# Kernel optimization log

Hardware: AMD Instinct MI355X
Metric: run time of the kernel (lower is better)

Reference implementation:

```python
import jax, jax.numpy as jnp
import numpy as np
import math

INPUT_SIZE = 1024
HIDDEN_SIZE = 1024
RANK = 256
BATCH = 32
SEQ = 512


def setup_inputs() -> dict:
    key = jax.random.key(0)
    k_x, k_a, k_b, k_c = jax.random.split(key, 4)
    stdv = 1.0 / math.sqrt(HIDDEN_SIZE)
    x = jax.random.normal(k_x, (BATCH, SEQ, INPUT_SIZE), dtype=jnp.float32)
    a = jax.random.uniform(k_a, (HIDDEN_SIZE, RANK * 4), minval=-stdv, maxval=stdv, dtype=jnp.float32)
    b = jax.random.uniform(k_b, (INPUT_SIZE, RANK * 4), minval=-stdv, maxval=stdv, dtype=jnp.float32)
    ct = jax.random.uniform(k_c, (RANK * 4, HIDDEN_SIZE), minval=-stdv, maxval=stdv, dtype=jnp.float32)
    return {"x": x, "a": a, "b": b, "ct": ct}


def reference(x, a, b, ct):
    B, S, _ = x.shape
    H = a.shape[0]
    R = a.shape[1] // 4
    ct3 = ct.reshape(4, R, H)  # (4, R, H)
    # Precompute input projection for all timesteps: (B, S, 4R)
    xb = jnp.einsum('bsi,ir->bsr', x, b)

    def step(carry, xb_t):
        h, c = carry
        g = (h @ a) * xb_t                      # (B, 4R)
        g = jnp.einsum('bkr,krh->bkh', g.reshape(B, 4, R), ct3)  # (B, 4, H)
        f_t = jax.nn.sigmoid(g[:, 0])
        i_t = jax.nn.sigmoid(g[:, 1])
        g_t = jnp.tanh(g[:, 2])
        o_t = jax.nn.sigmoid(g[:, 3])
        c = f_t * c + i_t * g_t
        h = o_t * jnp.tanh(c)
        return (h, c), h

    h0 = jnp.zeros((B, H), dtype=x.dtype)
    c0 = jnp.zeros((B, H), dtype=x.dtype)
    (h_t, c_t), hs = jax.lax.scan(step, (h0, c0), jnp.swapaxes(xb, 0, 1))
    hidden_seq = jnp.swapaxes(hs, 0, 1)  # (B, S, H)
    return hidden_seq, (h_t, c_t)
```

## Files before the change

### kernel.cpp

```cpp
#include <hip/hip_runtime.h>
#include <math.h>

#define NTHR 512

__device__ __forceinline__ void st_uc(float* p, float v) {
    asm volatile("global_store_dword %0, %1, off sc0 sc1" :: "v"(p), "v"(v) : "memory");
}
__device__ __forceinline__ void st_uc_u(unsigned* p, unsigned v) {
    asm volatile("global_store_dword %0, %1, off sc0 sc1" :: "v"(p), "v"(v) : "memory");
}
__device__ __forceinline__ float4 ld_uc4_nw(const float4* p) {
    float4 v;
    asm volatile("global_load_dwordx4 %0, %1, off sc0 sc1" : "=v"(v) : "v"(p) : "memory");
    return v;
}
__device__ __forceinline__ float ld_uc_nw(const float* p) {
    float v;
    asm volatile("global_load_dword %0, %1, off sc0 sc1" : "=v"(v) : "v"(p) : "memory");
    return v;
}
__device__ __forceinline__ void spin_tags64(const unsigned* base, int L, unsigned target) {
    const unsigned* p = base + L;
    for (;;) {
        unsigned v;
        asm volatile("global_load_dword %0, %1, off sc0 sc1\n\ts_waitcnt vmcnt(0)"
                     : "=v"(v) : "v"(p) : "memory");
        if (!__any((int)(v < target))) return;
        __builtin_amdgcn_s_sleep(1);
    }
}

__global__ void init_kernel(float* h_buf, unsigned* tags) {
    int i = blockIdx.x * blockDim.x + threadIdx.x;
    if (i < 65536) st_uc(h_buf + i, 0.0f);
    if (i < 1024) st_uc_u(tags + i, 0u);
}

__global__ __launch_bounds__(256) void xb_gemm(const float* __restrict__ X,
                                               const float* __restrict__ Bw,
                                               float* __restrict__ XB) {
    __shared__ float xs[16][132];
    __shared__ float bs[16][132];
    const int bm = blockIdx.x >> 3;
    const int bn = blockIdx.x & 7;
    const int m0 = bm * 128, n0 = bn * 128;
    const int tid = threadIdx.x;
    const int tx = tid & 15, ty = tid >> 4;
    float acc[8][8];
#pragma unroll
    for (int i = 0; i < 8; ++i)
#pragma unroll
        for (int j = 0; j < 8; ++j) acc[i][j] = 0.f;

    for (int k0 = 0; k0 < 1024; k0 += 16) {
#pragma unroll
        for (int p = 0; p < 2; ++p) {
            int f = tid + p * 256;
            int m = f >> 2, kq = f & 3;
            float4 v = *(const float4*)&X[(size_t)(m0 + m) * 1024 + k0 + kq * 4];
            xs[kq * 4 + 0][m] = v.x; xs[kq * 4 + 1][m] = v.y;
            xs[kq * 4 + 2][m] = v.z; xs[kq * 4 + 3][m] = v.w;
        }
#pragma unroll
        for (int p = 0; p < 2; ++p) {
            int f = tid + p * 256;
            int k = f >> 5, n = (f & 31) * 4;
            float4 v = *(const float4*)&Bw[(size_t)(k0 + k) * 1024 + n0 + n];
            *(float4*)&bs[k][n] = v;
        }
        __syncthreads();
#pragma unroll
        for (int k = 0; k < 16; ++k) {
            float xv[8], bv[8];
            *(float4*)&xv[0] = *(const float4*)&xs[k][ty * 8];
            *(float4*)&xv[4] = *(const float4*)&xs[k][ty * 8 + 4];
            *(float4*)&bv[0] = *(const float4*)&bs[k][tx * 8];
            *(float4*)&bv[4] = *(const float4*)&bs[k][tx * 8 + 4];
#pragma unroll
            for (int i = 0; i < 8; ++i)
#pragma unroll
                for (int j = 0; j < 8; ++j) acc[i][j] += xv[i] * bv[j];
        }
        __syncthreads();
    }
#pragma unroll
    for (int i = 0; i < 8; ++i)
#pragma unroll
        for (int j = 0; j < 8; j += 4) {
            float4 v = make_float4(acc[i][j], acc[i][j + 1], acc[i][j + 2], acc[i][j + 3]);
            *(float4*)&XB[(size_t)(m0 + ty * 8 + i) * 1024 + n0 + tx * 8 + j] = v;
        }
}

__global__ __launch_bounds__(NTHR, 1) void scan_kernel(
    const float* __restrict__ A, const float* __restrict__ CTm,
    float* __restrict__ XBH, float* __restrict__ h_buf, float* __restrict__ g_buf,
    float* __restrict__ ht_out, float* __restrict__ ct_out, unsigned* __restrict__ tags) {
    extern __shared__ float lds[];
    float* a_lf  = lds;
    float* ct_lf = lds + 16384;
    float* st0f  = lds + 32768;
    float* st1f  = lds + 36864;
    float4* lds4  = (float4*)lds;
    const float4* a_l4  = lds4;
    const float4* ct_l4 = lds4 + 4096;
    float4* st0_4 = lds4 + 8192;
    float4* st1_4 = lds4 + 9216;
    float* scr0 = st0f;
    float* scr1 = st1f;

    const int wg = blockIdx.x;
    const int bg0 = wg >> 6;
    const int bg1 = bg0 + 4;
    const int sg = wg & 63;
    const int c0wg = sg * 16;
    const int tid = threadIdx.x;

    {
        const int c = tid & 15, i0 = tid >> 4;
        for (int i = i0; i < 1024; i += 32) {
            a_lf[c * 1024 + i]  = A[(size_t)i * 1024 + c0wg + c];
            ct_lf[c * 1024 + i] = CTm[(size_t)i * 1024 + c0wg + c];
        }
    }

    const int L  = tid & 63;
    const int w  = tid >> 6;
    const int Lc = L & 7;
    const int Lb = (L >> 3) & 3;
    const int cg = w & 1, kq = w >> 1;

    int wIdx[8], sIdx[4];
#pragma unroll
    for (int c = 0; c < 8; ++c) wIdx[c] = (cg * 8 + (c ^ Lc)) * 256 + kq * 64 + L;
#pragma unroll
    for (int r = 0; r < 4; ++r) sIdx[r] = ((r ^ Lb) << 8) + kq * 64 + L;

    const int e_b   = L >> 4;
    const int e_j   = L & 15;
    const int e_cgo = e_j >> 3;
    const int e_sx  = e_b * 8 + (e_j & 7);
    const int col   = c0wg + e_j;

    float4* h4 = (float4*)h_buf;
    float4* g4 = (float4*)g_buf;

    float creg = 0.f;
    __syncthreads();

    auto sub = [&](int t, const unsigned* pollbase, unsigned polltgt,
                   const float4* src4, float4* st4, float* scr,
                   const float4* wmat, int epiw, bool isA, int bgx, float xbv) {
        if (w == 7) spin_tags64(pollbase, L, polltgt);
        __syncthreads();
        {
            float4 u0 = ld_uc4_nw(src4 + tid);
            float4 u1 = ld_uc4_nw(src4 + 512 + tid);
            asm volatile("s_waitcnt vmcnt(0)" ::: "memory");
            __builtin_amdgcn_sched_barrier(0);
            st4[tid] = u0; st4[512 + tid] = u1;
        }
        __syncthreads();
        float v[32];
        {
            float4 sv[4], wv[8];
#pragma unroll
            for (int r = 0; r < 4; ++r) sv[r] = st4[sIdx[r]];
#pragma unroll
            for (int c = 0; c < 8; ++c) wv[c] = wmat[wIdx[c]];
#pragma unroll
            for (int r = 0; r < 4; ++r)
#pragma unroll
                for (int c = 0; c < 8; ++c)
                    v[r * 8 + c] = sv[r].x * wv[c].x + sv[r].y * wv[c].y
                                 + sv[r].z * wv[c].z + sv[r].w * wv[c].w;
        }
#pragma unroll
        for (int j = 0; j < 16; ++j) v[j] = v[2 * j] + __shfl_xor(v[2 * j + 1], 1);
#pragma unroll
        for (int j = 0; j < 8; ++j)  v[j] = v[2 * j] + __shfl_xor(v[2 * j + 1], 2);
#pragma unroll
        for (int j = 0; j < 4; ++j)  v[j] = v[2 * j] + __shfl_xor(v[2 * j + 1], 4);
#pragma unroll
        for (int j = 0; j < 2; ++j)  v[j] = v[2 * j] + __shfl_xor(v[2 * j + 1], 8);
        v[0] = v[0] + __shfl_xor(v[1], 16);
        v[0] = v[0] + __shfl_xor(v[0], 32);
        __syncthreads();
        if (L < 32) scr[kq * 64 + cg * 32 + L] = v[0];
        __syncthreads();
        if (w == epiw) {
            asm volatile("s_waitcnt vmcnt(0)" ::: "memory");
            const int bglob = bgx * 4 + e_b;
            float q0 = scr[e_cgo * 32 + e_sx];
            float q1 = scr[64 + e_cgo * 32 + e_sx];
            float q2 = scr[128 + e_cgo * 32 + e_sx];
            float q3 = scr[192 + e_cgo * 32 + e_sx];
            if (isA) {
                float gv = (q0 + q1 + q2 + q3) * xbv;
                st_uc(g_buf + (t & 1) * 32768 + (size_t)bglob * 1024 + col, gv);
                asm volatile("s_waitcnt vmcnt(0)" ::: "memory");
                if (L == 0) st_uc_u(tags + bgx * 128 + 64 + sg, (unsigned)t + 1u);
            } else {
                float ft = 1.f / (1.f + __expf(-q0));
                float it = 1.f / (1.f + __expf(-q1));
                float gt = tanhf(q2);
                float ot = 1.f / (1.f + __expf(-q3));
                creg = ft * creg + it * gt;
                float hv = ot * tanhf(creg);
                st_uc(h_buf + (t & 1) * 32768 + (size_t)bglob * 1024 + col, hv);
                st_uc(XBH + ((size_t)bglob * 512 + t) * 1024 + col, hv);
                if (t == 511) {
                    st_uc(ht_out + (size_t)bglob * 1024 + col, hv);
                    st_uc(ct_out + (size_t)bglob * 1024 + col, creg);
                }
                asm volatile("s_waitcnt vmcnt(0)" ::: "memory");
                if (L == 0) st_uc_u(tags + bgx * 128 + sg, (unsigned)t + 1u);
            }
        }
    };

    for (int t = 0; t < 512; ++t) {
        const unsigned tu = (unsigned)t;
        float xb0 = 0.f, xb1 = 0.f;
        if (w == 0) xb0 = ld_uc_nw(XBH + ((size_t)(bg0 * 4 + e_b) * 512 + t) * 1024 + col);
        if (w == 4) xb1 = ld_uc_nw(XBH + ((size_t)(bg1 * 4 + e_b) * 512 + t) * 1024 + col);

        sub(t, tags + bg0 * 128, tu,
            h4 + ((t + 1) & 1) * 8192 + bg0 * 1024, st0_4, scr0, a_l4, 0, true, bg0, xb0);
        sub(t, tags + bg1 * 128, tu,
            h4 + ((t + 1) & 1) * 8192 + bg1 * 1024, st1_4, scr1, a_l4, 4, true, bg1, xb1);
        sub(t, tags + bg0 * 128 + 64, tu + 1u,
            g4 + (t & 1) * 8192 + bg0 * 1024, st0_4, scr0, ct_l4, 0, false, bg0, 0.f);
        sub(t, tags + bg1 * 128 + 64, tu + 1u,
            g4 + (t & 1) * 8192 + bg1 * 1024, st1_4, scr1, ct_l4, 4, false, bg1, 0.f);
    }
}

extern "C" void kernel_launch(void* const* d_in, const int* in_sizes, int n_in,
                              void* d_out, int out_size, void* d_ws, size_t ws_size,
                              hipStream_t stream) {
    const float* X   = (const float*)d_in[0];
    const float* A   = (const float*)d_in[1];
    const float* Bw  = (const float*)d_in[2];
    const float* CTm = (const float*)d_in[3];

    float* out    = (float*)d_out;
    float* XBH    = out;
    float* ht_out = out + (size_t)32 * 512 * 1024;
    float* ct_out = ht_out + 32 * 1024;

    float* h_buf = (float*)d_ws;
    float* g_buf = h_buf + 65536;
    unsigned* tags = (unsigned*)(g_buf + 65536);

    (void)hipFuncSetAttribute((const void*)scan_kernel,
                              hipFuncAttributeMaxDynamicSharedMemorySize, 163840);

    init_kernel<<<dim3(256), dim3(256), 0, stream>>>(h_buf, tags);
    xb_gemm<<<dim3(1024), dim3(256), 0, stream>>>(X, Bw, XBH);
    scan_kernel<<<dim3(256), dim3(NTHR), 163840, stream>>>(A, CTm, XBH, h_buf, g_buf,
                                                           ht_out, ct_out, tags);
}
```

Baseline: 4.868 ms.

## Software-pipeline scan substeps: prefetch next state during current matvec

Restructures the persistent scan loop so that the two batch groups' phases are interleaved (A0, B1 of previous step, B0, A1). Each substep polls and prefetches the next operand from global memory while the current LDS matvec runs. A single staging buffer is used and barriers are reduced. This targets the serialized poll→load→compute latency on every substep. In exchange the ordering is more complex, with a prologue and epilogue, which risks correctness or deadlock subtleties.

```diff
diff --git a/kernel.cpp b/kernel.cpp
--- a/kernel.cpp
+++ b/kernel.cpp
@@ -19,16 +19,7 @@
     asm volatile("global_load_dword %0, %1, off sc0 sc1" : "=v"(v) : "v"(p) : "memory");
     return v;
 }
-__device__ __forceinline__ void spin_tags64(const unsigned* base, int L, unsigned target) {
-    const unsigned* p = base + L;
-    for (;;) {
-        unsigned v;
-        asm volatile("global_load_dword %0, %1, off sc0 sc1\n\ts_waitcnt vmcnt(0)"
-                     : "=v"(v) : "v"(p) : "memory");
-        if (!__any((int)(v < target))) return;
-        __builtin_amdgcn_s_sleep(1);
-    }
-}
+#define VMCNT0 asm volatile("s_waitcnt vmcnt(0)" ::: "memory")
 
 __global__ void init_kernel(float* h_buf, unsigned* tags) {
     int i = blockIdx.x * blockDim.x + threadIdx.x;
@@ -99,22 +90,23 @@
     extern __shared__ float lds[];
     float* a_lf  = lds;
     float* ct_lf = lds + 16384;
-    float* st0f  = lds + 32768;
-    float* st1f  = lds + 36864;
-    float4* lds4  = (float4*)lds;
-    const float4* a_l4  = lds4;
-    const float4* ct_l4 = lds4 + 4096;
-    float4* st0_4 = lds4 + 8192;
-    float4* st1_4 = lds4 + 9216;
-    float* scr0 = st0f;
-    float* scr1 = st1f;
-
-    const int wg = blockIdx.x;
+    float* stgf  = lds + 32768;
+    float* scr0  = lds + 36864;
+    float* scr1  = lds + 37120;
+    const float4* a_l4  = (const float4*)a_lf;
+    const float4* ct_l4 = (const float4*)ct_lf;
+    float4* stg4 = (float4*)stgf;
+
+    const int wg  = blockIdx.x;
     const int bg0 = wg >> 6;
     const int bg1 = bg0 + 4;
-    const int sg = wg & 63;
+    const int sg  = wg & 63;
     const int c0wg = sg * 16;
     const int tid = threadIdx.x;
+    unsigned* tagH0 = tags + bg0 * 128;
+    unsigned* tagG0 = tagH0 + 64;
+    unsigned* tagH1 = tags + bg1 * 128;
+    unsigned* tagG1 = tagH1 + 64;
 
     {
         const int c = tid & 15, i0 = tid >> 4;
@@ -136,45 +128,50 @@
 #pragma unroll
     for (int r = 0; r < 4; ++r) sIdx[r] = ((r ^ Lb) << 8) + kq * 64 + L;
 
+    const int stag = (tid & 255) >> 2;
+
     const int e_b   = L >> 4;
     const int e_j   = L & 15;
     const int e_cgo = e_j >> 3;
     const int e_sx  = e_b * 8 + (e_j & 7);
     const int col   = c0wg + e_j;
 
-    float4* h4 = (float4*)h_buf;
-    float4* g4 = (float4*)g_buf;
+    const float4* h4 = (const float4*)h_buf;
+    const float4* g4 = (const float4*)g_buf;
 
     float creg = 0.f;
-    __syncthreads();
-
-    auto sub = [&](int t, const unsigned* pollbase, unsigned polltgt,
-                   const float4* src4, float4* st4, float* scr,
-                   const float4* wmat, int epiw, bool isA, int bgx, float xbv) {
-        if (w == 7) spin_tags64(pollbase, L, polltgt);
-        __syncthreads();
-        {
-            float4 u0 = ld_uc4_nw(src4 + tid);
-            float4 u1 = ld_uc4_nw(src4 + 512 + tid);
-            asm volatile("s_waitcnt vmcnt(0)" ::: "memory");
-            __builtin_amdgcn_sched_barrier(0);
-            st4[tid] = u0; st4[512 + tid] = u1;
-        }
-        __syncthreads();
+    float xbv = 0.f;
+    float4 pr0, pr1;
+
+    auto poll = [&](const unsigned* base, unsigned tgt) {
+        const unsigned* p = base + stag;
+        for (;;) {
+            unsigned vv;
+            asm volatile("global_load_dword %0, %1, off sc0 sc1\n\ts_waitcnt vmcnt(0)"
+                         : "=v"(vv) : "v"(p) : "memory");
+            if (!__any((int)(vv < tgt))) return;
+            __builtin_amdgcn_s_sleep(1);
+        }
+    };
+    auto subcore = [&](const float4* wmat, float* scr,
+                       const unsigned* pfb, unsigned pft, const float4* pfsrc, bool dopf) {
+        float4 sv[4], wv[8];
+#pragma unroll
+        for (int r = 0; r < 4; ++r) sv[r] = stg4[sIdx[r]];
+#pragma unroll
+        for (int c = 0; c < 8; ++c) wv[c] = wmat[wIdx[c]];
+        if (dopf) {
+            poll(pfb, pft);
+            pr0 = ld_uc4_nw(pfsrc + tid);
+            pr1 = ld_uc4_nw(pfsrc + 512 + tid);
+        }
         float v[32];
-        {
-            float4 sv[4], wv[8];
-#pragma unroll
-            for (int r = 0; r < 4; ++r) sv[r] = st4[sIdx[r]];
-#pragma unroll
-            for (int c = 0; c < 8; ++c) wv[c] = wmat[wIdx[c]];
-#pragma unroll
-            for (int r = 0; r < 4; ++r)
-#pragma unroll
-                for (int c = 0; c < 8; ++c)
-                    v[r * 8 + c] = sv[r].x * wv[c].x + sv[r].y * wv[c].y
-                                 + sv[r].z * wv[c].z + sv[r].w * wv[c].w;
-        }
+#pragma unroll
+        for (int r = 0; r < 4; ++r)
+#pragma unroll
+            for (int c = 0; c < 8; ++c)
+                v[r * 8 + c] = sv[r].x * wv[c].x + sv[r].y * wv[c].y
+                             + sv[r].z * wv[c].z + sv[r].w * wv[c].w;
 #pragma unroll
         for (int j = 0; j < 16; ++j) v[j] = v[2 * j] + __shfl_xor(v[2 * j + 1], 1);
 #pragma unroll
@@ -185,55 +182,106 @@
         for (int j = 0; j < 2; ++j)  v[j] = v[2 * j] + __shfl_xor(v[2 * j + 1], 8);
         v[0] = v[0] + __shfl_xor(v[1], 16);
         v[0] = v[0] + __shfl_xor(v[0], 32);
-        __syncthreads();
         if (L < 32) scr[kq * 64 + cg * 32 + L] = v[0];
-        __syncthreads();
-        if (w == epiw) {
-            asm volatile("s_waitcnt vmcnt(0)" ::: "memory");
-            const int bglob = bgx * 4 + e_b;
-            float q0 = scr[e_cgo * 32 + e_sx];
-            float q1 = scr[64 + e_cgo * 32 + e_sx];
-            float q2 = scr[128 + e_cgo * 32 + e_sx];
-            float q3 = scr[192 + e_cgo * 32 + e_sx];
-            if (isA) {
-                float gv = (q0 + q1 + q2 + q3) * xbv;
-                st_uc(g_buf + (t & 1) * 32768 + (size_t)bglob * 1024 + col, gv);
-                asm volatile("s_waitcnt vmcnt(0)" ::: "memory");
-                if (L == 0) st_uc_u(tags + bgx * 128 + 64 + sg, (unsigned)t + 1u);
+    };
+    auto epiA = [&](int t, float* scrS, int bgx, unsigned* tagGx) {
+        VMCNT0;
+        float q = scrS[e_cgo * 32 + e_sx] + scrS[64 + e_cgo * 32 + e_sx]
+                + scrS[128 + e_cgo * 32 + e_sx] + scrS[192 + e_cgo * 32 + e_sx];
+        st_uc(g_buf + (t & 1) * 32768 + (size_t)(bgx * 4 + e_b) * 1024 + col, q * xbv);
+        VMCNT0;
+        if (L == 0) st_uc_u(tagGx + sg, (unsigned)t + 1u);
+    };
+    auto epiB = [&](int t, float* scrS, int bgx, unsigned* tagHx) {
+        float q0 = scrS[e_cgo * 32 + e_sx],       q1 = scrS[64 + e_cgo * 32 + e_sx];
+        float q2 = scrS[128 + e_cgo * 32 + e_sx], q3 = scrS[192 + e_cgo * 32 + e_sx];
+        float ft = 1.f / (1.f + __expf(-q0));
+        float it = 1.f / (1.f + __expf(-q1));
+        float gt = tanhf(q2);
+        float ot = 1.f / (1.f + __expf(-q3));
+        creg = ft * creg + it * gt;
+        float hv = ot * tanhf(creg);
+        int bglob = bgx * 4 + e_b;
+        st_uc(h_buf + (t & 1) * 32768 + (size_t)bglob * 1024 + col, hv);
+        st_uc(XBH + ((size_t)bglob * 512 + t) * 1024 + col, hv);
+        if (t == 511) {
+            st_uc(ht_out + (size_t)bglob * 1024 + col, hv);
+            st_uc(ct_out + (size_t)bglob * 1024 + col, creg);
+        }
+        VMCNT0;
+        if (L == 0) st_uc_u(tagHx + sg, (unsigned)t + 1u);
+    };
+
+    __syncthreads();
+    {
+        const float4* s = h4 + 8192 + (size_t)bg0 * 1024;
+        pr0 = ld_uc4_nw(s + tid);
+        pr1 = ld_uc4_nw(s + 512 + tid);
+        VMCNT0;
+        stg4[tid] = pr0; stg4[512 + tid] = pr1;
+        __syncthreads();
+    }
+
+    for (int k = 0; k < 512; ++k) {
+        if (w == 1) xbv = ld_uc_nw(XBH + ((size_t)(bg0 * 4 + e_b) * 512 + k) * 1024 + col);
+        if (w == 2) xbv = ld_uc_nw(XBH + ((size_t)(bg1 * 4 + e_b) * 512 + k) * 1024 + col);
+
+        subcore(a_l4, scr0, tagG1, (unsigned)k,
+                g4 + ((k + 1) & 1) * 8192 + (size_t)bg1 * 1024, true);
+        __syncthreads();
+        if (w == 1) epiA(k, scr0, bg0, tagG0);
+        VMCNT0;
+        stg4[tid] = pr0; stg4[512 + tid] = pr1;
+        __syncthreads();
+
+        {
+            const float4* srcn = g4 + (k & 1) * 8192 + (size_t)bg0 * 1024;
+            if (k > 0) {
+                subcore(ct_l4, scr1, tagG0, (unsigned)k + 1u, srcn, true);
             } else {
-                float ft = 1.f / (1.f + __expf(-q0));
-                float it = 1.f / (1.f + __expf(-q1));
-                float gt = tanhf(q2);
-                float ot = 1.f / (1.f + __expf(-q3));
-                creg = ft * creg + it * gt;
-                float hv = ot * tanhf(creg);
-                st_uc(h_buf + (t & 1) * 32768 + (size_t)bglob * 1024 + col, hv);
-                st_uc(XBH + ((size_t)bglob * 512 + t) * 1024 + col, hv);
-                if (t == 511) {
-                    st_uc(ht_out + (size_t)bglob * 1024 + col, hv);
-                    st_uc(ct_out + (size_t)bglob * 1024 + col, creg);
-                }
-                asm volatile("s_waitcnt vmcnt(0)" ::: "memory");
-                if (L == 0) st_uc_u(tags + bgx * 128 + sg, (unsigned)t + 1u);
+                poll(tagG0, 1u);
+                pr0 = ld_uc4_nw(srcn + tid);
+                pr1 = ld_uc4_nw(srcn + 512 + tid);
             }
-        }
-    };
-
-    for (int t = 0; t < 512; ++t) {
-        const unsigned tu = (unsigned)t;
-        float xb0 = 0.f, xb1 = 0.f;
-        if (w == 0) xb0 = ld_uc_nw(XBH + ((size_t)(bg0 * 4 + e_b) * 512 + t) * 1024 + col);
-        if (w == 4) xb1 = ld_uc_nw(XBH + ((size_t)(bg1 * 4 + e_b) * 512 + t) * 1024 + col);
-
-        sub(t, tags + bg0 * 128, tu,
-            h4 + ((t + 1) & 1) * 8192 + bg0 * 1024, st0_4, scr0, a_l4, 0, true, bg0, xb0);
-        sub(t, tags + bg1 * 128, tu,
-            h4 + ((t + 1) & 1) * 8192 + bg1 * 1024, st1_4, scr1, a_l4, 4, true, bg1, xb1);
-        sub(t, tags + bg0 * 128 + 64, tu + 1u,
-            g4 + (t & 1) * 8192 + bg0 * 1024, st0_4, scr0, ct_l4, 0, false, bg0, 0.f);
-        sub(t, tags + bg1 * 128 + 64, tu + 1u,
-            g4 + (t & 1) * 8192 + bg1 * 1024, st1_4, scr1, ct_l4, 4, false, bg1, 0.f);
-    }
+            __syncthreads();
+            if (k > 0 && w == 4) epiB(k - 1, scr1, bg1, tagH1);
+            VMCNT0;
+            stg4[tid] = pr0; stg4[512 + tid] = pr1;
+            __syncthreads();
+        }
+
+        subcore(ct_l4, scr0, tagH1, (unsigned)k,
+                h4 + ((k + 1) & 1) * 8192 + (size_t)bg1 * 1024, true);
+        __syncthreads();
+        if (w == 0) epiB(k, scr0, bg0, tagH0);
+        VMCNT0;
+        stg4[tid] = pr0; stg4[512 + tid] = pr1;
+        __syncthreads();
+
+        {
+            bool pf = (k < 511);
+            subcore(a_l4, scr1, tagH0, (unsigned)k + 1u,
+                    h4 + (k & 1) * 8192 + (size_t)bg0 * 1024, pf);
+            __syncthreads();
+            if (w == 2) epiA(k, scr1, bg1, tagG1);
+            VMCNT0;
+            if (pf) { stg4[tid] = pr0; stg4[512 + tid] = pr1; }
+            __syncthreads();
+        }
+    }
+
+    poll(tagG1, 512u);
+    {
+        const float4* s = g4 + 8192 + (size_t)bg1 * 1024;
+        pr0 = ld_uc4_nw(s + tid);
+        pr1 = ld_uc4_nw(s + 512 + tid);
+    }
+    VMCNT0;
+    stg4[tid] = pr0; stg4[512 + tid] = pr1;
+    __syncthreads();
+    subcore(ct_l4, scr1, tagG1, 0u, g4, false);
+    __syncthreads();
+    if (w == 4) epiB(511, scr1, bg1, tagH1);
 }
 
 extern "C" void kernel_launch(void* const* d_in, const int* in_sizes, int n_in,
@@ -254,10 +302,10 @@
     unsigned* tags = (unsigned*)(g_buf + 65536);
 
     (void)hipFuncSetAttribute((const void*)scan_kernel,
-                              hipFuncAttributeMaxDynamicSharedMemorySize, 163840);
+                              hipFuncAttributeMaxDynamicSharedMemorySize, 149504);
 
     init_kernel<<<dim3(256), dim3(256), 0, stream>>>(h_buf, tags);
     xb_gemm<<<dim3(1024), dim3(256), 0, stream>>>(X, Bw, XBH);
-    scan_kernel<<<dim3(256), dim3(NTHR), 163840, stream>>>(A, CTm, XBH, h_buf, g_buf,
+    scan_kernel<<<dim3(256), dim3(NTHR), 149504, stream>>>(A, CTm, XBH, h_buf, g_buf,
                                                            ht_out, ct_out, tags);
 }
```

Result: slower. 5.823 ms (+19.6%).

## Replace tag-based flags with step-tagged 64-bit packed values and deferred epilogues

Applied to the files above, without the earlier changes.

Each h and g element is now stored as a 64-bit word that packs the timestep tag with the float value. Consumers spin directly on the data they need, which removes the separate tag array, the flag-store round trip and the extra waitcnt fences. Epilogue work (the gate nonlinearities and g production) is moved into the polling window of the next sub-step, so it overlaps with waiting, and some barriers are dropped. In exchange, global traffic on the exchange buffers doubles (64-bit per element) and every thread polls eight atomic loads instead of one wave polling tags.

```diff
diff --git a/kernel.cpp b/kernel.cpp
--- a/kernel.cpp
+++ b/kernel.cpp
@@ -2,38 +2,18 @@
 #include <math.h>
 
 #define NTHR 512
+typedef unsigned long long u64;
 
 __device__ __forceinline__ void st_uc(float* p, float v) {
     asm volatile("global_store_dword %0, %1, off sc0 sc1" :: "v"(p), "v"(v) : "memory");
 }
-__device__ __forceinline__ void st_uc_u(unsigned* p, unsigned v) {
-    asm volatile("global_store_dword %0, %1, off sc0 sc1" :: "v"(p), "v"(v) : "memory");
-}
-__device__ __forceinline__ float4 ld_uc4_nw(const float4* p) {
-    float4 v;
-    asm volatile("global_load_dwordx4 %0, %1, off sc0 sc1" : "=v"(v) : "v"(p) : "memory");
-    return v;
-}
-__device__ __forceinline__ float ld_uc_nw(const float* p) {
-    float v;
-    asm volatile("global_load_dword %0, %1, off sc0 sc1" : "=v"(v) : "v"(p) : "memory");
-    return v;
-}
-__device__ __forceinline__ void spin_tags64(const unsigned* base, int L, unsigned target) {
-    const unsigned* p = base + L;
-    for (;;) {
-        unsigned v;
-        asm volatile("global_load_dword %0, %1, off sc0 sc1\n\ts_waitcnt vmcnt(0)"
-                     : "=v"(v) : "v"(p) : "memory");
-        if (!__any((int)(v < target))) return;
-        __builtin_amdgcn_s_sleep(1);
-    }
-}
-
-__global__ void init_kernel(float* h_buf, unsigned* tags) {
+
+__global__ void init_kernel(u64* hp, u64* gp) {
     int i = blockIdx.x * blockDim.x + threadIdx.x;
-    if (i < 65536) st_uc(h_buf + i, 0.0f);
-    if (i < 1024) st_uc_u(tags + i, 0u);
+    if (i < 65536) {
+        __hip_atomic_store(hp + i, 0xFFFFFFFF00000000ull, __ATOMIC_RELAXED, __HIP_MEMORY_SCOPE_AGENT);
+        __hip_atomic_store(gp + i, 0xFFFFFFFE00000000ull, __ATOMIC_RELAXED, __HIP_MEMORY_SCOPE_AGENT);
+    }
 }
 
 __global__ __launch_bounds__(256) void xb_gemm(const float* __restrict__ X,
@@ -94,25 +74,22 @@
 
 __global__ __launch_bounds__(NTHR, 1) void scan_kernel(
     const float* __restrict__ A, const float* __restrict__ CTm,
-    float* __restrict__ XBH, float* __restrict__ h_buf, float* __restrict__ g_buf,
-    float* __restrict__ ht_out, float* __restrict__ ct_out, unsigned* __restrict__ tags) {
+    float* __restrict__ XBH, u64* __restrict__ hp, u64* __restrict__ gp,
+    float* __restrict__ ht_out, float* __restrict__ ct_out) {
     extern __shared__ float lds[];
     float* a_lf  = lds;
     float* ct_lf = lds + 16384;
-    float* st0f  = lds + 32768;
-    float* st1f  = lds + 36864;
-    float4* lds4  = (float4*)lds;
-    const float4* a_l4  = lds4;
-    const float4* ct_l4 = lds4 + 4096;
-    float4* st0_4 = lds4 + 8192;
-    float4* st1_4 = lds4 + 9216;
-    float* scr0 = st0f;
-    float* scr1 = st1f;
-
-    const int wg = blockIdx.x;
+    float* stgf  = lds + 32768;
+    float* scr0  = lds + 36864;
+    float* scr1  = lds + 37120;
+    const float4* a_l4  = (const float4*)a_lf;
+    const float4* ct_l4 = (const float4*)ct_lf;
+    float4* stg4 = (float4*)stgf;
+
+    const int wg  = blockIdx.x;
     const int bg0 = wg >> 6;
     const int bg1 = bg0 + 4;
-    const int sg = wg & 63;
+    const int sg  = wg & 63;
     const int c0wg = sg * 16;
     const int tid = threadIdx.x;
 
@@ -142,39 +119,22 @@
     const int e_sx  = e_b * 8 + (e_j & 7);
     const int col   = c0wg + e_j;
 
-    float4* h4 = (float4*)h_buf;
-    float4* g4 = (float4*)g_buf;
-
     float creg = 0.f;
-    __syncthreads();
-
-    auto sub = [&](int t, const unsigned* pollbase, unsigned polltgt,
-                   const float4* src4, float4* st4, float* scr,
-                   const float4* wmat, int epiw, bool isA, int bgx, float xbv) {
-        if (w == 7) spin_tags64(pollbase, L, polltgt);
-        __syncthreads();
-        {
-            float4 u0 = ld_uc4_nw(src4 + tid);
-            float4 u1 = ld_uc4_nw(src4 + 512 + tid);
-            asm volatile("s_waitcnt vmcnt(0)" ::: "memory");
-            __builtin_amdgcn_sched_barrier(0);
-            st4[tid] = u0; st4[512 + tid] = u1;
-        }
-        __syncthreads();
+    float xbv  = 0.f;
+
+    auto compute = [&](const float4* wmat, float* scr) {
+        float4 sv[4], wv[8];
+#pragma unroll
+        for (int r = 0; r < 4; ++r) sv[r] = stg4[sIdx[r]];
+#pragma unroll
+        for (int c = 0; c < 8; ++c) wv[c] = wmat[wIdx[c]];
         float v[32];
-        {
-            float4 sv[4], wv[8];
-#pragma unroll
-            for (int r = 0; r < 4; ++r) sv[r] = st4[sIdx[r]];
-#pragma unroll
-            for (int c = 0; c < 8; ++c) wv[c] = wmat[wIdx[c]];
-#pragma unroll
-            for (int r = 0; r < 4; ++r)
-#pragma unroll
-                for (int c = 0; c < 8; ++c)
-                    v[r * 8 + c] = sv[r].x * wv[c].x + sv[r].y * wv[c].y
-                                 + sv[r].z * wv[c].z + sv[r].w * wv[c].w;
-        }
+#pragma unroll
+        for (int r = 0; r < 4; ++r)
+#pragma unroll
+            for (int c = 0; c < 8; ++c)
+                v[r * 8 + c] = sv[r].x * wv[c].x + sv[r].y * wv[c].y
+                             + sv[r].z * wv[c].z + sv[r].w * wv[c].w;
 #pragma unroll
         for (int j = 0; j < 16; ++j) v[j] = v[2 * j] + __shfl_xor(v[2 * j + 1], 1);
 #pragma unroll
@@ -185,55 +145,82 @@
         for (int j = 0; j < 2; ++j)  v[j] = v[2 * j] + __shfl_xor(v[2 * j + 1], 8);
         v[0] = v[0] + __shfl_xor(v[1], 16);
         v[0] = v[0] + __shfl_xor(v[0], 32);
-        __syncthreads();
         if (L < 32) scr[kq * 64 + cg * 32 + L] = v[0];
-        __syncthreads();
-        if (w == epiw) {
-            asm volatile("s_waitcnt vmcnt(0)" ::: "memory");
-            const int bglob = bgx * 4 + e_b;
-            float q0 = scr[e_cgo * 32 + e_sx];
-            float q1 = scr[64 + e_cgo * 32 + e_sx];
-            float q2 = scr[128 + e_cgo * 32 + e_sx];
-            float q3 = scr[192 + e_cgo * 32 + e_sx];
-            if (isA) {
-                float gv = (q0 + q1 + q2 + q3) * xbv;
-                st_uc(g_buf + (t & 1) * 32768 + (size_t)bglob * 1024 + col, gv);
-                asm volatile("s_waitcnt vmcnt(0)" ::: "memory");
-                if (L == 0) st_uc_u(tags + bgx * 128 + 64 + sg, (unsigned)t + 1u);
-            } else {
-                float ft = 1.f / (1.f + __expf(-q0));
-                float it = 1.f / (1.f + __expf(-q1));
-                float gt = tanhf(q2);
-                float ot = 1.f / (1.f + __expf(-q3));
-                creg = ft * creg + it * gt;
-                float hv = ot * tanhf(creg);
-                st_uc(h_buf + (t & 1) * 32768 + (size_t)bglob * 1024 + col, hv);
-                st_uc(XBH + ((size_t)bglob * 512 + t) * 1024 + col, hv);
-                if (t == 511) {
-                    st_uc(ht_out + (size_t)bglob * 1024 + col, hv);
-                    st_uc(ct_out + (size_t)bglob * 1024 + col, creg);
-                }
-                asm volatile("s_waitcnt vmcnt(0)" ::: "memory");
-                if (L == 0) st_uc_u(tags + bgx * 128 + sg, (unsigned)t + 1u);
-            }
-        }
-    };
-
-    for (int t = 0; t < 512; ++t) {
-        const unsigned tu = (unsigned)t;
-        float xb0 = 0.f, xb1 = 0.f;
-        if (w == 0) xb0 = ld_uc_nw(XBH + ((size_t)(bg0 * 4 + e_b) * 512 + t) * 1024 + col);
-        if (w == 4) xb1 = ld_uc_nw(XBH + ((size_t)(bg1 * 4 + e_b) * 512 + t) * 1024 + col);
-
-        sub(t, tags + bg0 * 128, tu,
-            h4 + ((t + 1) & 1) * 8192 + bg0 * 1024, st0_4, scr0, a_l4, 0, true, bg0, xb0);
-        sub(t, tags + bg1 * 128, tu,
-            h4 + ((t + 1) & 1) * 8192 + bg1 * 1024, st1_4, scr1, a_l4, 4, true, bg1, xb1);
-        sub(t, tags + bg0 * 128 + 64, tu + 1u,
-            g4 + (t & 1) * 8192 + bg0 * 1024, st0_4, scr0, ct_l4, 0, false, bg0, 0.f);
-        sub(t, tags + bg1 * 128 + 64, tu + 1u,
-            g4 + (t & 1) * 8192 + bg1 * 1024, st1_4, scr1, ct_l4, 4, false, bg1, 0.f);
-    }
+    };
+
+    auto epiA_fn = [&](int t, const float* s, int bgx) {
+        float q = s[e_cgo * 32 + e_sx] + s[64 + e_cgo * 32 + e_sx]
+                + s[128 + e_cgo * 32 + e_sx] + s[192 + e_cgo * 32 + e_sx];
+        u64 pk = ((u64)(unsigned)t << 32) | (u64)__float_as_uint(q * xbv);
+        __hip_atomic_store(gp + (size_t)(t & 1) * 32768 + (size_t)(bgx * 4 + e_b) * 1024 + col,
+                           pk, __ATOMIC_RELAXED, __HIP_MEMORY_SCOPE_AGENT);
+    };
+    auto epiB_fn = [&](int t, const float* s, int bgx) {
+        float q0 = s[e_cgo * 32 + e_sx],       q1 = s[64 + e_cgo * 32 + e_sx];
+        float q2 = s[128 + e_cgo * 32 + e_sx], q3 = s[192 + e_cgo * 32 + e_sx];
+        float ft = 1.f / (1.f + __expf(-q0));
+        float it = 1.f / (1.f + __expf(-q1));
+        float gt = tanhf(q2);
+        float ot = 1.f / (1.f + __expf(-q3));
+        creg = ft * creg + it * gt;
+        float hv = ot * tanhf(creg);
+        int bglob = bgx * 4 + e_b;
+        u64 pk = ((u64)(unsigned)t << 32) | (u64)__float_as_uint(hv);
+        __hip_atomic_store(hp + (size_t)(t & 1) * 32768 + (size_t)bglob * 1024 + col,
+                           pk, __ATOMIC_RELAXED, __HIP_MEMORY_SCOPE_AGENT);
+        st_uc(XBH + ((size_t)bglob * 512 + t) * 1024 + col, hv);
+        if (t == 511) {
+            st_uc(ht_out + (size_t)bglob * 1024 + col, hv);
+            st_uc(ct_out + (size_t)bglob * 1024 + col, creg);
+        }
+    };
+
+    auto sub = [&](const u64* base, unsigned expect, const float4* wmat, float* scr,
+                   int ek, int t) {
+        const u64* src = base + tid;
+        u64 q[8];
+#pragma unroll
+        for (int j = 0; j < 8; ++j)
+            q[j] = __hip_atomic_load(src + 512 * j, __ATOMIC_RELAXED, __HIP_MEMORY_SCOPE_AGENT);
+        if (ek == 1) { if (w == 4 && t > 0) epiB_fn(t - 1, scr1, bg1); }
+        else if (ek == 2) { if (w == 1) epiA_fn(t, scr0, bg0); }
+        else if (ek == 3) { if (w == 2) epiA_fn(t, scr1, bg1); }
+        else if (ek == 4) { if (w == 0) epiB_fn(t, scr0, bg0); }
+        for (;;) {
+            bool ok = true;
+#pragma unroll
+            for (int j = 0; j < 8; ++j) ok &= ((unsigned)(q[j] >> 32) == expect);
+            if (!__any(!ok)) break;
+            __builtin_amdgcn_s_sleep(1);
+#pragma unroll
+            for (int j = 0; j < 8; ++j)
+                q[j] = __hip_atomic_load(src + 512 * j, __ATOMIC_RELAXED, __HIP_MEMORY_SCOPE_AGENT);
+        }
+#pragma unroll
+        for (int j = 0; j < 8; ++j) stgf[tid + 512 * j] = __uint_as_float((unsigned)q[j]);
+        __syncthreads();
+        compute(wmat, scr);
+        __syncthreads();
+    };
+
+    __syncthreads();
+
+    for (int k = 0; k < 512; ++k) {
+        const unsigned expA = (unsigned)(k - 1);
+        const unsigned expB = (unsigned)k;
+        if (w == 1) xbv = __uint_as_float(__hip_atomic_load(
+            (const unsigned*)(XBH + ((size_t)(bg0 * 4 + e_b) * 512 + k) * 1024 + col),
+            __ATOMIC_RELAXED, __HIP_MEMORY_SCOPE_AGENT));
+        if (w == 2) xbv = __uint_as_float(__hip_atomic_load(
+            (const unsigned*)(XBH + ((size_t)(bg1 * 4 + e_b) * 512 + k) * 1024 + col),
+            __ATOMIC_RELAXED, __HIP_MEMORY_SCOPE_AGENT));
+
+        sub(hp + (size_t)((k + 1) & 1) * 32768 + (size_t)bg0 * 4096, expA, a_l4, scr0, 1, k);
+        sub(hp + (size_t)((k + 1) & 1) * 32768 + (size_t)bg1 * 4096, expA, a_l4, scr1, 2, k);
+        sub(gp + (size_t)(k & 1) * 32768 + (size_t)bg0 * 4096, expB, ct_l4, scr0, 3, k);
+        sub(gp + (size_t)(k & 1) * 32768 + (size_t)bg1 * 4096, expB, ct_l4, scr1, 4, k);
+    }
+    if (w == 4) epiB_fn(511, scr1, bg1);
 }
 
 extern "C" void kernel_launch(void* const* d_in, const int* in_sizes, int n_in,
@@ -249,15 +236,14 @@
     float* ht_out = out + (size_t)32 * 512 * 1024;
     float* ct_out = ht_out + 32 * 1024;
 
-    float* h_buf = (float*)d_ws;
-    float* g_buf = h_buf + 65536;
-    unsigned* tags = (unsigned*)(g_buf + 65536);
+    u64* hp = (u64*)d_ws;
+    u64* gp = hp + 65536;
 
     (void)hipFuncSetAttribute((const void*)scan_kernel,
-                              hipFuncAttributeMaxDynamicSharedMemorySize, 163840);
-
-    init_kernel<<<dim3(256), dim3(256), 0, stream>>>(h_buf, tags);
+                              hipFuncAttributeMaxDynamicSharedMemorySize, 149504);
+
+    init_kernel<<<dim3(256), dim3(256), 0, stream>>>(hp, gp);
     xb_gemm<<<dim3(1024), dim3(256), 0, stream>>>(X, Bw, XBH);
-    scan_kernel<<<dim3(256), dim3(NTHR), 163840, stream>>>(A, CTm, XBH, h_buf, g_buf,
-                                                           ht_out, ct_out, tags);
-}
+    scan_kernel<<<dim3(256), dim3(NTHR), 149504, stream>>>(A, CTm, XBH, hp, gp,
+                                                           ht_out, ct_out);
+}
```

After: 4.759 ms. 1.02x faster.
